# Performance work log

Measured on AMD Instinct MI355X. Metric: run time of the kernel, lower is better.

The kernel has to match this reference:

```python
import jax, jax.numpy as jnp
import numpy as np

N_NODES = 48758
REL_NUM = 5
BN_EPS = 1e-5


def _dan(h, edge_index, edge_type, win_w, win_b, wrel, cout_w, cout_b):
    # One DAN layer: gather -> gcn-norm scatter-sum + per-relation transform -> scatter-softmax -> scatter-sum.
    dst, src = edge_index[0], edge_index[1]
    xlin = h @ win_w + win_b                         # [N, D]
    x_j = xlin[src]                                  # [E, D] per-edge gather
    # gcn_norm(edge_index, add_self_loops=False): deg over col (= edge_index[1])
    ones = jnp.ones(src.shape[0], xlin.dtype)
    deg = jax.ops.segment_sum(ones, src, num_segments=N_NODES)
    dis = jnp.where(deg > 0, 1.0 / jnp.sqrt(deg), 0.0)
    norm = dis[dst] * dis[src]                       # [E]
    msg_gcn = jax.ops.segment_sum(x_j * norm[:, None], dst, num_segments=N_NODES)
    # per-relation linear transform on edge messages (small fixed relation loop)
    res = jnp.zeros_like(x_j)
    for r in range(REL_NUM):
        res = res + jnp.where((edge_type == r)[:, None], x_j @ wrel[r], 0.0)
    # scatter-softmax over destination-node neighborhoods, per feature channel
    m = jax.ops.segment_max(res, dst, num_segments=N_NODES)      # [N, D]
    e = jnp.exp(res - m[dst])
    s = jax.ops.segment_sum(e, dst, num_segments=N_NODES)
    weig = e / s[dst]
    msg = jax.ops.segment_sum(res * weig, dst, num_segments=N_NODES)
    return (msg_gcn + 0.1 * jax.nn.relu(msg)) @ cout_w + cout_b


def setup_inputs() -> dict:
    key = jax.random.key(0)
    ks = jax.random.split(key, 18)
    D = 128
    E = 750000
    s = 0.05
    inp = {}
    inp['x'] = jax.random.normal(ks[0], (N_NODES, D), jnp.float32)
    inp['edge_index'] = jax.random.randint(ks[1], (2, E), 0, N_NODES)
    inp['edge_type'] = jax.random.randint(ks[2], (E,), 0, REL_NUM)
    inp['edge_weight'] = jax.random.uniform(ks[3], (E,), jnp.float32)
    inp['idx'] = jax.random.randint(ks[4], (4096,), 0, N_NODES)
    # input projection + batchnorm params
    inp['proj_w'] = jax.random.normal(ks[5], (D, D), jnp.float32) * s
    inp['proj_b'] = jnp.zeros((D,), jnp.float32)
    inp['bn_g'] = jnp.ones((D,), jnp.float32)
    inp['bn_b'] = jnp.zeros((D,), jnp.float32)
    # two DAN layers (hidden=output=128)
    inp['win0_w'] = jax.random.normal(ks[6], (D, D), jnp.float32) * s
    inp['win0_b'] = jnp.zeros((D,), jnp.float32)
    inp['wrel0'] = jax.random.normal(ks[7], (REL_NUM, D, D), jnp.float32) * s
    inp['cout0_w'] = jax.random.normal(ks[8], (D, D), jnp.float32) * s
    inp['cout0_b'] = jnp.zeros((D,), jnp.float32)
    inp['win1_w'] = jax.random.normal(ks[9], (D, D), jnp.float32) * s
    inp['win1_b'] = jnp.zeros((D,), jnp.float32)
    inp['wrel1'] = jax.random.normal(ks[10], (REL_NUM, D, D), jnp.float32) * s
    inp['cout1_w'] = jax.random.normal(ks[11], (D, D), jnp.float32) * s
    inp['cout1_b'] = jnp.zeros((D,), jnp.float32)
    return inp


def reference(x, edge_index, edge_type, edge_weight, idx,
              proj_w, proj_b, bn_g, bn_b,
              win0_w, win0_b, wrel0, cout0_w, cout0_b,
              win1_w, win1_b, wrel1, cout1_w, cout1_b):
    # proj -> BatchNorm1d (training-mode batch stats) -> relu
    h = x @ proj_w + proj_b
    mu = jnp.mean(h, axis=0)
    var = jnp.mean(jnp.square(h - mu), axis=0)
    h = (h - mu) / jnp.sqrt(var + BN_EPS) * bn_g + bn_b
    h = jax.nn.relu(h)
    h = _dan(h, edge_index, edge_type, win0_w, win0_b, wrel0, cout0_w, cout0_b)
    h = _dan(h, edge_index, edge_type, win1_w, win1_b, wrel1, cout1_w, cout1_b)
    h = jax.nn.gelu(h, approximate=False)  # dropout is identity for reference
    return h[idx]
```

## Files before the change

kernel.cpp:

```cpp
#include <hip/hip_runtime.h>

#define HIST_BPG 32
#define HIST_B   (HIST_BPG * 4)
#define HIST_MAXW 12288

__device__ inline float bf2f(unsigned short u) {
    return __uint_as_float(((unsigned)u) << 16);
}
__device__ inline unsigned short f2bf(float f) {
    unsigned u = __float_as_uint(f);
    u += 0x7fffu + ((u >> 16) & 1u);
    return (unsigned short)(u >> 16);
}

__device__ inline int xcd_swizzle(int bid, int n)
{
    const int NX = 8;
    int q = n / NX, r = n % NX;
    int xcd = bid % NX;
    int rank = bid / NX;
    return (xcd < r) ? xcd * (q + 1) + rank : r * (q + 1) + (xcd - r) * q + rank;
}

typedef __attribute__((ext_vector_type(8))) short short8v;
typedef __attribute__((ext_vector_type(4))) float f32x4;


__device__ __forceinline__
void gemmf32_body(const float* __restrict__ A, const float* __restrict__ W,
                  const float* __restrict__ bias, float* __restrict__ C,
                  unsigned short* __restrict__ Ct, int M, int tile)
{
    __shared__ float As[64][132];
    __shared__ float Ws[32][128];

    const int tid = threadIdx.x;
    const int row0 = tile * 64;

#pragma unroll
    for (int i = 0; i < 8; ++i) {
        int idx = tid + i * 256;
        int rr = idx >> 5;
        int cc = (idx & 31) << 2;
        int gr = row0 + rr;
        float4 v = make_float4(0.f, 0.f, 0.f, 0.f);
        if (gr < M) v = *reinterpret_cast<const float4*>(A + (size_t)gr * 128 + cc);
        *reinterpret_cast<float4*>(&As[rr][cc]) = v;
    }

    const int tx = tid & 15;
    const int ty = tid >> 4;
    float acc[4][8];
#pragma unroll
    for (int i = 0; i < 4; ++i)
#pragma unroll
        for (int j = 0; j < 8; ++j) acc[i][j] = 0.f;

    for (int kt = 0; kt < 4; ++kt) {
        __syncthreads();
#pragma unroll
        for (int i = 0; i < 4; ++i) {
            int idx = tid + i * 256;
            int rr = idx >> 5;
            int cc = (idx & 31) << 2;
            *reinterpret_cast<float4*>(&Ws[rr][cc]) =
                *reinterpret_cast<const float4*>(W + (size_t)(kt * 32 + rr) * 128 + cc);
        }
        __syncthreads();
#pragma unroll
        for (int kk = 0; kk < 32; ++kk) {
            const int k = kt * 32 + kk;
            float a0 = As[ty * 4 + 0][k];
            float a1 = As[ty * 4 + 1][k];
            float a2 = As[ty * 4 + 2][k];
            float a3 = As[ty * 4 + 3][k];
            float w[8];
#pragma unroll
            for (int j = 0; j < 8; ++j) w[j] = Ws[kk][tx + 16 * j];
#pragma unroll
            for (int j = 0; j < 8; ++j) {
                acc[0][j] = fmaf(a0, w[j], acc[0][j]);
                acc[1][j] = fmaf(a1, w[j], acc[1][j]);
                acc[2][j] = fmaf(a2, w[j], acc[2][j]);
                acc[3][j] = fmaf(a3, w[j], acc[3][j]);
            }
        }
    }

    float bb[8];
#pragma unroll
    for (int j = 0; j < 8; ++j) bb[j] = bias ? bias[tx + 16 * j] : 0.f;

#pragma unroll
    for (int i = 0; i < 4; ++i) {
        int gr = row0 + ty * 4 + i;
        if (gr >= M) continue;
#pragma unroll
        for (int j = 0; j < 8; ++j) {
            float v = acc[i][j] + bb[j];
            if (C)  C[(size_t)gr * 128 + tx + 16 * j] = v;
            if (Ct) Ct[(size_t)(tx + 16 * j) * 128 + gr] = f2bf(v);
        }
    }
}

__device__ __forceinline__
void mfmaw_body(const unsigned short* __restrict__ A,
                const unsigned short* __restrict__ Wmat,
                const float* __restrict__ bias,
                float* __restrict__ Cf, unsigned short* __restrict__ Cb,
                int M, int tile)
{
    __shared__ unsigned short Bs[16384];

    const int tid = threadIdx.x;
#pragma unroll
    for (int i = 0; i < 4; ++i) {
        int idx = tid + i * 512;
        uint4 v = *reinterpret_cast<const uint4*>(Wmat + (size_t)idx * 8);
        int row = idx >> 4;
        int j = idx & 15;
        int byte = row * 256 + ((j ^ (row & 15)) << 4);
        *reinterpret_cast<uint4*>(reinterpret_cast<char*>(Bs) + byte) = v;
    }

    const int wave = tid >> 6;
    const int lane = tid & 63;
    const int grp = lane >> 4;
    const int l16 = lane & 15;
    const int row = tile * 128 + wave * 16 + l16;
    const int rc = row < M ? row : M - 1;

    short8v a[4];
#pragma unroll
    for (int kt = 0; kt < 4; ++kt)
        a[kt] = *reinterpret_cast<const short8v*>(A + (size_t)rc * 128 + kt * 32 + grp * 8);

    __syncthreads();

    f32x4 acc[8] = {};
#pragma unroll
    for (int kt = 0; kt < 4; ++kt) {
        const int joff = kt * 4 + grp;
#pragma unroll
        for (int n = 0; n < 8; ++n) {
            int brow = 16 * n + l16;
            int byte = brow * 256 + ((joff ^ (brow & 15)) << 4);
            short8v b = *reinterpret_cast<const short8v*>(
                reinterpret_cast<const char*>(Bs) + byte);
            acc[n] = __builtin_amdgcn_mfma_f32_16x16x32_bf16(b, a[kt], acc[n], 0, 0, 0);
        }
    }

    if (row >= M) return;

    float4 bb[8];
#pragma unroll
    for (int n = 0; n < 8; ++n)
        bb[n] = bias ? *reinterpret_cast<const float4*>(bias + 16 * n + grp * 4)
                     : make_float4(0.f, 0.f, 0.f, 0.f);

#pragma unroll
    for (int n = 0; n < 8; ++n) {
        float v0 = acc[n][0] + bb[n].x;
        float v1 = acc[n][1] + bb[n].y;
        float v2 = acc[n][2] + bb[n].z;
        float v3 = acc[n][3] + bb[n].w;
        if (Cf) {
            *reinterpret_cast<float4*>(Cf + (size_t)row * 128 + 16 * n + grp * 4) =
                make_float4(v0, v1, v2, v3);
        }
        if (Cb) {
            unsigned u0 = (unsigned)f2bf(v0) | ((unsigned)f2bf(v1) << 16);
            unsigned u1 = (unsigned)f2bf(v2) | ((unsigned)f2bf(v3) << 16);
            *reinterpret_cast<uint2*>(Cb + (size_t)row * 128 + 16 * n + grp * 4) =
                make_uint2(u0, u1);
        }
    }
}

__device__ void fused_dispatch(const unsigned short* A, const unsigned short* Wt,
                               const float* biasbuf, unsigned short* Xb,
                               unsigned short* Yb, int base, int M, int nmats,
                               int bid, int nF)
{
    int w = xcd_swizzle(bid, nF);
    int m = w % nmats;
    int tile = w / nmats;
    unsigned short* out = (m == 0) ? Xb : Yb + (size_t)(m - 1) * (size_t)M * 128;
    mfmaw_body(A, Wt + (size_t)(base + m) * 16384,
               biasbuf + (size_t)(base + m) * 128, nullptr, out, M, tile);
}

__device__ void biasprod_body(const float* __restrict__ v, const float* __restrict__ W,
                              const float* __restrict__ add, float* __restrict__ out)
{
    int t = threadIdx.x;
    if (t >= 128) return;
    float s = add ? add[t] : 0.f;
    for (int j = 0; j < 128; ++j) s = fmaf(v[j], W[(size_t)j * 128 + t], s);
    out[t] = s;
}

__device__ void wtconv_body(const float* __restrict__ W, unsigned short* __restrict__ O)
{
    for (int i = threadIdx.x; i < 16384; i += 256) {
        int k = i >> 7, n = i & 127;
        O[(size_t)n * 128 + k] = f2bf(W[i]);
    }
}

__device__ void bn_stats_body(const float* __restrict__ h, float* __restrict__ sums,
                              int Nn, int b)
{
    const int c = threadIdx.x & 127;
    const int half = threadIdx.x >> 7;
    float s = 0.f, q = 0.f;
    for (int row = b * 2 + half; row < Nn; row += 512) {
        float v = h[(size_t)row * 128 + c];
        s += v;
        q += v * v;
    }
    __shared__ float ls[256], lq[256];
    ls[threadIdx.x] = s;
    lq[threadIdx.x] = q;
    __syncthreads();
    if (half == 0) {
        s += ls[threadIdx.x + 128];
        q += lq[threadIdx.x + 128];
        atomicAdd(&sums[c], s);
        atomicAdd(&sums[128 + c], q);
    }
}

__device__ void scan_block_sums_body(const int* __restrict__ cnt, int* __restrict__ bsum,
                                     int Nn, int b)
{
    __shared__ int sd[256];
    int tid = threadIdx.x;
    int i = b * 256 + tid;
    sd[tid] = i < Nn ? ((cnt[i] + 3) & ~3) : 0;
    __syncthreads();
#pragma unroll
    for (int s = 128; s > 0; s >>= 1) {
        if (tid < s) sd[tid] += sd[tid + s];
        __syncthreads();
    }
    if (tid == 0) bsum[b] = sd[0];
}

__device__ void scan_offsets_body(int* __restrict__ bsum, int nb)
{
    __shared__ int sd[256];
    int tid = threadIdx.x;
    int v = tid < nb ? bsum[tid] : 0;
    sd[tid] = v;
    __syncthreads();
    for (int d = 1; d < 256; d <<= 1) {
        int t = tid >= d ? sd[tid - d] : 0;
        __syncthreads();
        sd[tid] += t;
        __syncthreads();
    }
    if (tid < nb) bsum[tid] = sd[tid] - v;
}


__global__ __launch_bounds__(256)
void hist_kernel(const int* __restrict__ ei, unsigned* __restrict__ partial,
                 int Nn, int E, int WORDS, int HALFR)
{
    __shared__ unsigned sh[HIST_MAXW];
    const int hbid = blockIdx.x;
    const int g = hbid / HIST_BPG;
    const int j = hbid - g * HIST_BPG;

    for (int w = threadIdx.x; w < WORDS; w += 256) sh[w] = 0;
    __syncthreads();

    const int* col = (g < 2) ? (ei + E) : ei;
    const int base = (g & 1) * HALFR;
    const size_t e0 = (size_t)E * j / HIST_BPG;
    const size_t e1 = (size_t)E * (j + 1) / HIST_BPG;
    for (size_t e = e0 + threadIdx.x; e < e1; e += 256) {
        int n = col[e] - base;
        if ((unsigned)n < (unsigned)HALFR)
            atomicAdd(&sh[n >> 1], 1u << ((n & 1) * 16));
    }
    __syncthreads();

    unsigned* out = partial + (size_t)hbid * WORDS;
    for (int w = threadIdx.x; w < WORDS; w += 256) out[w] = sh[w];
}

__global__ __launch_bounds__(256)
void kprod1(const float* win0w, const float* win0b, const float* win1w, const float* win1b,
            const float* cout0w, const float* cout0b, const float* cout1w,
            const float* cout1b, const float* wrel0,
            const float* x, const float* proj_w, const float* proj_b,
            unsigned short* xb, float* WfA1, unsigned short* Wt, float* biasbuf,
            int nrel, size_t nx4)
{
    const int IA1 = 1 + nrel, IC1 = 2 + 2 * nrel, IPRJ = 3 + 2 * nrel;
    const int nProd = 1 + nrel;
    int bid = blockIdx.x;
    if (bid < 2 * nProd) {
        int p = bid >> 1, tile = bid & 1;
        if (p == 0)
            gemmf32_body(cout0w, win1w, nullptr, WfA1, Wt + (size_t)IA1 * 16384, 128, tile);
        else
            gemmf32_body(win0w, wrel0 + (size_t)(p - 1) * 16384, nullptr,
                         nullptr, Wt + (size_t)p * 16384, 128, tile);
        return;
    }
    bid -= 2 * nProd;
    if (bid < nProd) {
        if (bid == 0) biasprod_body(cout0b, win1w, win1b, biasbuf + (size_t)IA1 * 128);
        else biasprod_body(win0b, wrel0 + (size_t)(bid - 1) * 16384, nullptr,
                           biasbuf + (size_t)bid * 128);
        return;
    }
    bid -= nProd;
    if (bid == 0) { wtconv_body(win0w, Wt); return; }
    if (bid == 1) { wtconv_body(cout1w, Wt + (size_t)IC1 * 16384); return; }
    if (bid == 2) { wtconv_body(proj_w, Wt + (size_t)IPRJ * 16384); return; }
    if (bid == 3) {
        int t = threadIdx.x;
        if (t < 128) {
            biasbuf[t] = win0b[t];
            biasbuf[(size_t)IC1 * 128 + t] = cout1b[t];
            biasbuf[(size_t)IPRJ * 128 + t] = proj_b[t];
        }
        return;
    }
    size_t i = (size_t)(bid - 4) * 256 + threadIdx.x;
    if (i < nx4) {
        float4 v = reinterpret_cast<const float4*>(x)[i];
        ushort4 pk = make_ushort4(f2bf(v.x), f2bf(v.y), f2bf(v.z), f2bf(v.w));
        reinterpret_cast<ushort4*>(xb)[i] = pk;
    }
}

__global__ __launch_bounds__(512)
void kproj(const unsigned short* xb, const unsigned short* Wt, const float* biasbuf,
           float* h, int mat, int M)
{
    mfmaw_body(xb, Wt + (size_t)mat * 16384, biasbuf + (size_t)mat * 128,
               h, nullptr, M, blockIdx.x);
}

__global__ __launch_bounds__(256)
void k2_reduce_bnstats(const unsigned* __restrict__ partial, float* __restrict__ dis,
                       int* __restrict__ cnt, const float* __restrict__ h,
                       float* __restrict__ bnsums, int Nn, int WORDS, int HALFR, int nRed)
{
    int bid = blockIdx.x;
    if (bid < nRed) {
        int t = bid * 256 + threadIdx.x;
        if (t < 4 * WORDS) {
            int histo = t / (2 * WORDS);
            int rem = t - histo * 2 * WORDS;
            int half = rem / WORDS;
            int w = rem - half * WORDS;
            int g = histo * 2 + half;
            unsigned slo = 0, shi = 0;
            const unsigned* p = partial + (size_t)(g * HIST_BPG) * WORDS + w;
#pragma unroll 4
            for (int j = 0; j < HIST_BPG; ++j) {
                unsigned u = p[(size_t)j * WORDS];
                slo += u & 0xffffu;
                shi += u >> 16;
            }
            int n0 = half * HALFR + 2 * w;
            int n1 = n0 + 1;
            if (histo == 0) {
                if (n0 < Nn) dis[n0] = slo ? rsqrtf((float)slo) : 0.f;
                if (n1 < Nn) dis[n1] = shi ? rsqrtf((float)shi) : 0.f;
            } else {
                if (n0 < Nn) cnt[n0] = (int)slo;
                if (n1 < Nn) cnt[n1] = (int)shi;
            }
        }
        return;
    }
    bn_stats_body(h, bnsums, Nn, bid - nRed);
}

__global__ __launch_bounds__(256)
void k3_prod2_bnfin_scan1(const float* wrel1, const float* WfA1,
                          unsigned short* Wt, float* biasbuf, int nrel,
                          const float* __restrict__ sums, const float* __restrict__ g,
                          const float* __restrict__ b, float* __restrict__ sc,
                          const int* __restrict__ cnt, int* __restrict__ bsum, int Nn)
{
    const int IA1 = 1 + nrel, IB1 = 2 + nrel;
    int bid = blockIdx.x;
    if (bid < 2 * nrel) {
        int p = bid >> 1, tile = bid & 1;
        gemmf32_body(WfA1, wrel1 + (size_t)p * 16384, nullptr,
                     nullptr, Wt + (size_t)(IB1 + p) * 16384, 128, tile);
        return;
    }
    bid -= 2 * nrel;
    if (bid < nrel) {
        biasprod_body(biasbuf + (size_t)IA1 * 128, wrel1 + (size_t)bid * 16384, nullptr,
                      biasbuf + (size_t)(IB1 + bid) * 128);
        return;
    }
    bid -= nrel;
    if (bid == 0) {
        int c = threadIdx.x;
        if (c < 128) {
            float inv = 1.f / (float)Nn;
            float mu = sums[c] * inv;
            float var = sums[128 + c] * inv - mu * mu;
            float rstd = rsqrtf(var + 1e-5f);
            float scale = rstd * g[c];
            sc[c] = scale;
            sc[128 + c] = b[c] - mu * scale;
        }
        return;
    }
    scan_block_sums_body(cnt, bsum, Nn, bid - 1);
}

__global__ __launch_bounds__(256)
void k4_scanoff_bnapply(int* __restrict__ bsum, int nb,
                        const float* __restrict__ h, const float* __restrict__ sc,
                        unsigned short* __restrict__ hb, size_t n4)
{
    if (blockIdx.x == 0) { scan_offsets_body(bsum, nb); return; }
    size_t i = (size_t)(blockIdx.x - 1) * 256 + threadIdx.x;
    if (i >= n4) return;
    int c = (int)(i & 31) << 2;
    float4 v = reinterpret_cast<const float4*>(h)[i];
    float o0 = fmaxf(fmaf(v.x, sc[c + 0], sc[128 + c + 0]), 0.f);
    float o1 = fmaxf(fmaf(v.y, sc[c + 1], sc[128 + c + 1]), 0.f);
    float o2 = fmaxf(fmaf(v.z, sc[c + 2], sc[128 + c + 2]), 0.f);
    float o3 = fmaxf(fmaf(v.w, sc[c + 3], sc[128 + c + 3]), 0.f);
    ushort4 pk = make_ushort4(f2bf(o0), f2bf(o1), f2bf(o2), f2bf(o3));
    reinterpret_cast<ushort4*>(hb)[i] = pk;
}

__global__ __launch_bounds__(256)
void k4b_scanfinal(const int* __restrict__ cnt, const int* __restrict__ bsum,
                   int* __restrict__ rowptr, int* __restrict__ cursor,
                   uint4* __restrict__ csr, unsigned* __restrict__ Yw,
                   unsigned sink_woff, int Nn, int nb)
{
    if ((int)blockIdx.x == nb) {
        int t = threadIdx.x;
        if (t < 64) Yw[sink_woff + t] = 0xC2C8C2C8u;
        return;
    }
    __shared__ int sd[256];
    int tid = threadIdx.x;
    int b = blockIdx.x;
    int i = b * 256 + tid;
    int v = i < Nn ? cnt[i] : 0;
    int pv = (v + 3) & ~3;
    sd[tid] = pv;
    __syncthreads();
    for (int d = 1; d < 256; d <<= 1) {
        int t2 = tid >= d ? sd[tid - d] : 0;
        __syncthreads();
        sd[tid] += t2;
        __syncthreads();
    }
    if (i < Nn) {
        int off = sd[tid] - pv + bsum[b];
        rowptr[i] = off;
        cursor[i] = off;
        uint4 sink = make_uint4(0u, sink_woff, 0u, 0u);
        for (int j = v; j < pv; ++j) csr[off + j] = sink;
        if (i == Nn - 1) {
            rowptr[Nn] = off + pv;
            for (int q = 0; q < 8; ++q) csr[off + pv + q] = sink;
        }
    }
}

__global__ __launch_bounds__(512)
void k5_mfma_scatter(const unsigned short* hb, const unsigned short* Wt,
                     const float* biasbuf, unsigned short* Xb, unsigned short* Yb,
                     int M, int nmats, int nF,
                     const int* __restrict__ ei, const int* __restrict__ et,
                     const float* __restrict__ dis, int* __restrict__ cursor,
                     uint4* __restrict__ csr, int E, int Nn, int nS)
{
    const int minv = nF < nS ? nF : nS;
    int bid = blockIdx.x;
    int fIdx = -1, sIdx = -1;
    if (bid < 2 * minv) {
        if (bid & 1) fIdx = bid >> 1; else sIdx = bid >> 1;
    } else {
        int rem = bid - 2 * minv;
        if (nF > nS) fIdx = minv + rem; else sIdx = minv + rem;
    }
    if (sIdx >= 0) {
        int e = sIdx * 512 + threadIdx.x;
        if (e < E) {
            int dst = ei[e];
            int src = ei[E + e];
            int pos = atomicAdd(&cursor[dst], 1);
            float nrm = dis[dst] * dis[src];
            csr[pos] = make_uint4((unsigned)(src * 64),
                                  (unsigned)((et[e] * Nn + src) * 64),
                                  __float_as_uint(nrm), 0u);
        }
        return;
    }
    fused_dispatch(hb, Wt, biasbuf, Xb, Yb, 0, M, nmats, fIdx, nF);
}

__global__ __launch_bounds__(512)
void k_fusedpass(const unsigned short* A, const unsigned short* Wt, const float* biasbuf,
                 unsigned short* Xb, unsigned short* Yb, int base, int M, int nmats,
                 int nF)
{
    fused_dispatch(A, Wt, biasbuf, Xb, Yb, base, M, nmats, blockIdx.x, nF);
}

__global__ __launch_bounds__(512)
void k_cout_gelu(const unsigned short* __restrict__ A, const unsigned short* Wt,
                 const float* biasbuf, float* __restrict__ out, int mat, int M)
{
    const unsigned short* Wmat = Wt + (size_t)mat * 16384;
    const float* bias = biasbuf + (size_t)mat * 128;

    __shared__ unsigned short Bs[16384];
    const int tid = threadIdx.x;
#pragma unroll
    for (int i = 0; i < 4; ++i) {
        int idx = tid + i * 512;
        uint4 v = *reinterpret_cast<const uint4*>(Wmat + (size_t)idx * 8);
        int row = idx >> 4;
        int j = idx & 15;
        int byte = row * 256 + ((j ^ (row & 15)) << 4);
        *reinterpret_cast<uint4*>(reinterpret_cast<char*>(Bs) + byte) = v;
    }

    const int wave = tid >> 6;
    const int lane = tid & 63;
    const int grp = lane >> 4;
    const int l16 = lane & 15;
    const int row = blockIdx.x * 128 + wave * 16 + l16;
    const int rc = row < M ? row : M - 1;

    short8v a[4];
#pragma unroll
    for (int kt = 0; kt < 4; ++kt)
        a[kt] = *reinterpret_cast<const short8v*>(A + (size_t)rc * 128 + kt * 32 + grp * 8);

    __syncthreads();

    f32x4 acc[8] = {};
#pragma unroll
    for (int kt = 0; kt < 4; ++kt) {
        const int joff = kt * 4 + grp;
#pragma unroll
        for (int n = 0; n < 8; ++n) {
            int brow = 16 * n + l16;
            int byte = brow * 256 + ((joff ^ (brow & 15)) << 4);
            short8v b = *reinterpret_cast<const short8v*>(
                reinterpret_cast<const char*>(Bs) + byte);
            acc[n] = __builtin_amdgcn_mfma_f32_16x16x32_bf16(b, a[kt], acc[n], 0, 0, 0);
        }
    }

    if (row >= M) return;

    const float kg = 0.7071067811865475f;
#pragma unroll
    for (int n = 0; n < 8; ++n) {
        float4 bb = *reinterpret_cast<const float4*>(bias + 16 * n + grp * 4);
        float v0 = acc[n][0] + bb.x;
        float v1 = acc[n][1] + bb.y;
        float v2 = acc[n][2] + bb.z;
        float v3 = acc[n][3] + bb.w;
        v0 = 0.5f * v0 * (1.f + erff(v0 * kg));
        v1 = 0.5f * v1 * (1.f + erff(v1 * kg));
        v2 = 0.5f * v2 * (1.f + erff(v2 * kg));
        v3 = 0.5f * v3 * (1.f + erff(v3 * kg));
        *reinterpret_cast<float4*>(out + (size_t)row * 128 + 16 * n + grp * 4) =
            make_float4(v0, v1, v2, v3);
    }
}

__global__ __launch_bounds__(256)
void node_gather(const int* __restrict__ rowptr, const uint4* __restrict__ csr,
                 const unsigned* __restrict__ Xw, const unsigned* __restrict__ Yw,
                 unsigned short* __restrict__ outb,
                 const int* __restrict__ idxmap, int count)
{
    int gid = blockIdx.x * 4 + (threadIdx.x >> 6);
    if (gid >= count) return;
    int node = idxmap ? idxmap[gid] : gid;
    int lane = threadIdx.x & 63;

    int i = rowptr[node];
    const int end = rowptr[node + 1];

    float mg0 = 0.f, mg1 = 0.f, s0 = 0.f, s1 = 0.f, t0 = 0.f, t1 = 0.f;

    if (i < end) {
        uint4 cur[4];
#pragma unroll
        for (int q = 0; q < 4; ++q) cur[q] = csr[i + q];

        for (; i < end; i += 4) {
            uint4 nxt[4];
#pragma unroll
            for (int q = 0; q < 4; ++q) nxt[q] = csr[i + 4 + q];

            unsigned xp[4], yp[4];
#pragma unroll
            for (int q = 0; q < 4; ++q) {
                xp[q] = Xw[cur[q].x + lane];
                yp[q] = Yw[cur[q].y + lane];
            }
#pragma unroll
            for (int q = 0; q < 4; ++q) {
                float nrm = __uint_as_float(cur[q].z);
                float x0 = bf2f((unsigned short)(xp[q] & 0xffffu));
                float x1 = bf2f((unsigned short)(xp[q] >> 16));
                float y0 = bf2f((unsigned short)(yp[q] & 0xffffu));
                float y1 = bf2f((unsigned short)(yp[q] >> 16));
                float w0 = __expf(y0), w1 = __expf(y1);
                mg0 = fmaf(x0, nrm, mg0);
                mg1 = fmaf(x1, nrm, mg1);
                s0 += w0; s1 += w1;
                t0 = fmaf(y0, w0, t0);
                t1 = fmaf(y1, w1, t1);
            }
#pragma unroll
            for (int q = 0; q < 4; ++q) cur[q] = nxt[q];
        }
    }

    float o0 = mg0 + 0.1f * fmaxf(s0 > 0.f ? t0 / s0 : 0.f, 0.f);
    float o1 = mg1 + 0.1f * fmaxf(s1 > 0.f ? t1 / s1 : 0.f, 0.f);
    unsigned pk = (unsigned)f2bf(o0) | ((unsigned)f2bf(o1) << 16);
    *reinterpret_cast<unsigned*>(outb + (size_t)gid * 128 + (lane << 1)) = pk;
}

extern "C" void kernel_launch(void* const* d_in, const int* in_sizes, int n_in,
                              void* d_out, int out_size, void* d_ws, size_t ws_size,
                              hipStream_t stream)
{
    const float* x      = (const float*)d_in[0];
    const int*   ei     = (const int*)d_in[1];
    const int*   et     = (const int*)d_in[2];
    const int*   idxp   = (const int*)d_in[4];
    const float* proj_w = (const float*)d_in[5];
    const float* proj_b = (const float*)d_in[6];
    const float* bn_g   = (const float*)d_in[7];
    const float* bn_b   = (const float*)d_in[8];
    const float* win_w[2]  = {(const float*)d_in[9],  (const float*)d_in[14]};
    const float* win_b[2]  = {(const float*)d_in[10], (const float*)d_in[15]};
    const float* wrel[2]   = {(const float*)d_in[11], (const float*)d_in[16]};
    const float* cout_w[2] = {(const float*)d_in[12], (const float*)d_in[17]};
    const float* cout_b[2] = {(const float*)d_in[13], (const float*)d_in[18]};

    const int Nn  = in_sizes[0] / 128;
    const int E   = in_sizes[1] / 2;
    const int Mo  = in_sizes[4];
    const int nrel = in_sizes[11] / (128 * 128);
    const size_t ND = (size_t)Nn * 128;

    const int HALFR = ((Nn + 3) / 4) * 2;
    const int WORDS = HALFR / 2;
    if (WORDS > HIST_MAXW) return;

    const int IA1 = 1 + nrel;
    const int IC1 = 2 + 2 * nrel;
    const int IPRJ = 3 + 2 * nrel;
    const int NMATS = 4 + 2 * nrel;

    char* p = (char*)d_ws;
    float* h    = (float*)p;                  p += ND * 4;
    unsigned short* hb = (unsigned short*)p;  p += ND * 2;
    unsigned short* xb = (unsigned short*)p;  p += ND * 2;
    unsigned short* Xb = (unsigned short*)p;  p += ND * 2;
    unsigned short* Yb = (unsigned short*)p;  p += (size_t)nrel * ND * 2 + 256;
    unsigned short* msgb = (unsigned short*)p; p += ND * 2;
    unsigned short* Wt = (unsigned short*)p;  p += (size_t)NMATS * 16384 * 2;
    float* WfA1 = (float*)p;                  p += (size_t)16384 * 4;
    float* biasbuf = (float*)p;               p += (size_t)NMATS * 128 * 4;
    uint4* csr  = (uint4*)p;                  p += ((size_t)E + 3 * (size_t)Nn + 16) * 16;
    unsigned* partial = (unsigned*)p;         p += (size_t)HIST_B * WORDS * 4;
    float* dis  = (float*)p;                  p += (size_t)Nn * 4;
    int*   cnt  = (int*)p;                    p += (size_t)Nn * 4;
    int*   rowptr = (int*)p;                  p += ((size_t)Nn + 1) * 4;
    int*   cursor = (int*)p;                  p += (size_t)Nn * 4;
    int*   bsum = (int*)p;                    p += 1024 * 4;
    float* bnsums = (float*)p;                p += 256 * 4;
    float* bnsc   = (float*)p;                p += 256 * 4;
    if ((size_t)(p - (char*)d_ws) > ws_size) return;

    const unsigned sink_woff = (unsigned)((size_t)nrel * Nn * 64);

    const int tiles128 = (Nn + 127) / 128;
    const size_t n4 = ND / 4;
    const int n4grid = (int)((n4 + 255) / 256);
    const int nb = (Nn + 255) / 256;
    const int nRed = (4 * WORDS + 255) / 256;
    const int nS = (E + 511) / 512;
    const int nmats = 1 + nrel;
    const int nFused = nmats * tiles128;
    const int nConv = (int)((n4 + 255) / 256);

    hipMemsetAsync(bnsums, 0, 256 * 4, stream);

    hist_kernel<<<HIST_B, 256, 0, stream>>>(ei, partial, Nn, E, WORDS, HALFR);

    kprod1<<<2 * (1 + nrel) + (1 + nrel) + 4 + nConv, 256, 0, stream>>>(
        win_w[0], win_b[0], win_w[1], win_b[1], cout_w[0], cout_b[0],
        cout_w[1], cout_b[1], wrel[0], x, proj_w, proj_b,
        xb, WfA1, Wt, biasbuf, nrel, n4);

    kproj<<<tiles128, 512, 0, stream>>>(xb, Wt, biasbuf, h, IPRJ, Nn);

    k2_reduce_bnstats<<<nRed + 256, 256, 0, stream>>>(
        partial, dis, cnt, h, bnsums, Nn, WORDS, HALFR, nRed);

    k3_prod2_bnfin_scan1<<<3 * nrel + 1 + nb, 256, 0, stream>>>(
        wrel[1], WfA1, Wt, biasbuf, nrel,
        bnsums, bn_g, bn_b, bnsc, cnt, bsum, Nn);

    k4_scanoff_bnapply<<<1 + n4grid, 256, 0, stream>>>(bsum, nb, h, bnsc, hb, n4);

    k4b_scanfinal<<<nb + 1, 256, 0, stream>>>(cnt, bsum, rowptr, cursor, csr,
                                              (unsigned*)Yb, sink_woff, Nn, nb);

    k5_mfma_scatter<<<nFused + nS, 512, 0, stream>>>(
        hb, Wt, biasbuf, Xb, Yb, Nn, nmats, nFused,
        ei, et, dis, cursor, csr, E, Nn, nS);

    node_gather<<<(Nn + 3) / 4, 256, 0, stream>>>(
        rowptr, csr, (const unsigned*)Xb, (const unsigned*)Yb, msgb, nullptr, Nn);

    k_fusedpass<<<nFused, 512, 0, stream>>>(msgb, Wt, biasbuf, Xb, Yb, IA1, Nn,
                                            nmats, nFused);

    node_gather<<<(Mo + 3) / 4, 256, 0, stream>>>(
        rowptr, csr, (const unsigned*)Xb, (const unsigned*)Yb, msgb, idxp, Mo);

    k_cout_gelu<<<(Mo + 127) / 128, 512, 0, stream>>>(
        msgb, Wt, biasbuf, (float*)d_out, IC1, Mo);
}
```

Before: 291.9 us.

## Interleave relation outputs per node, use exp2 with prescaled weights, fuse hist reduce

The per-relation Y outputs are stored interleaved per source node ([src][rel][128]) instead of relation-major, and the CSR offsets are updated to match. This is meant to improve locality when node_gather reads messages. Relation weights and biases are prescaled by log2(e) so the gather can use exp2f, with a ln2 factor applied at the output. The histogram reduction moves into the projection kernel launch, separate from the BN stats pass, which changes launch grouping.

```diff
diff --git a/kernel.cpp b/kernel.cpp
--- a/kernel.cpp
+++ b/kernel.cpp
@@ -3,6 +3,8 @@
 #define HIST_BPG 32
 #define HIST_B   (HIST_BPG * 4)
 #define HIST_MAXW 12288
+#define LOG2E 1.4426950408889634f
+#define LN2   0.6931471805599453f
 
 __device__ inline float bf2f(unsigned short u) {
     return __uint_as_float(((unsigned)u) << 16);
@@ -29,7 +31,7 @@
 __device__ __forceinline__
 void gemmf32_body(const float* __restrict__ A, const float* __restrict__ W,
                   const float* __restrict__ bias, float* __restrict__ C,
-                  unsigned short* __restrict__ Ct, int M, int tile)
+                  unsigned short* __restrict__ Ct, int M, int tile, float scale)
 {
     __shared__ float As[64][132];
     __shared__ float Ws[32][128];
@@ -97,7 +99,7 @@
         if (gr >= M) continue;
 #pragma unroll
         for (int j = 0; j < 8; ++j) {
-            float v = acc[i][j] + bb[j];
+            float v = (acc[i][j] + bb[j]) * scale;
             if (C)  C[(size_t)gr * 128 + tx + 16 * j] = v;
             if (Ct) Ct[(size_t)(tx + 16 * j) * 128 + gr] = f2bf(v);
         }
@@ -109,7 +111,7 @@
                 const unsigned short* __restrict__ Wmat,
                 const float* __restrict__ bias,
                 float* __restrict__ Cf, unsigned short* __restrict__ Cb,
-                int M, int tile)
+                int ldcb, int M, int tile)
 {
     __shared__ unsigned short Bs[16384];
 
@@ -173,7 +175,7 @@
         if (Cb) {
             unsigned u0 = (unsigned)f2bf(v0) | ((unsigned)f2bf(v1) << 16);
             unsigned u1 = (unsigned)f2bf(v2) | ((unsigned)f2bf(v3) << 16);
-            *reinterpret_cast<uint2*>(Cb + (size_t)row * 128 + 16 * n + grp * 4) =
+            *reinterpret_cast<uint2*>(Cb + (size_t)row * ldcb + 16 * n + grp * 4) =
                 make_uint2(u0, u1);
         }
     }
@@ -187,19 +189,21 @@
     int w = xcd_swizzle(bid, nF);
     int m = w % nmats;
     int tile = w / nmats;
-    unsigned short* out = (m == 0) ? Xb : Yb + (size_t)(m - 1) * (size_t)M * 128;
+    unsigned short* out = (m == 0) ? Xb : Yb + (size_t)(m - 1) * 128;
+    int ldcb = (m == 0) ? 128 : (nmats - 1) * 128;
     mfmaw_body(A, Wt + (size_t)(base + m) * 16384,
-               biasbuf + (size_t)(base + m) * 128, nullptr, out, M, tile);
+               biasbuf + (size_t)(base + m) * 128, nullptr, out, ldcb, M, tile);
 }
 
 __device__ void biasprod_body(const float* __restrict__ v, const float* __restrict__ W,
-                              const float* __restrict__ add, float* __restrict__ out)
+                              const float* __restrict__ add, float* __restrict__ out,
+                              float scale)
 {
     int t = threadIdx.x;
     if (t >= 128) return;
     float s = add ? add[t] : 0.f;
     for (int j = 0; j < 128; ++j) s = fmaf(v[j], W[(size_t)j * 128 + t], s);
-    out[t] = s;
+    out[t] = s * scale;
 }
 
 __device__ void wtconv_body(const float* __restrict__ W, unsigned short* __restrict__ O)
@@ -307,17 +311,18 @@
     if (bid < 2 * nProd) {
         int p = bid >> 1, tile = bid & 1;
         if (p == 0)
-            gemmf32_body(cout0w, win1w, nullptr, WfA1, Wt + (size_t)IA1 * 16384, 128, tile);
+            gemmf32_body(cout0w, win1w, nullptr, WfA1, Wt + (size_t)IA1 * 16384,
+                         128, tile, 1.f);
         else
             gemmf32_body(win0w, wrel0 + (size_t)(p - 1) * 16384, nullptr,
-                         nullptr, Wt + (size_t)p * 16384, 128, tile);
+                         nullptr, Wt + (size_t)p * 16384, 128, tile, LOG2E);
         return;
     }
     bid -= 2 * nProd;
     if (bid < nProd) {
-        if (bid == 0) biasprod_body(cout0b, win1w, win1b, biasbuf + (size_t)IA1 * 128);
+        if (bid == 0) biasprod_body(cout0b, win1w, win1b, biasbuf + (size_t)IA1 * 128, 1.f);
         else biasprod_body(win0b, wrel0 + (size_t)(bid - 1) * 16384, nullptr,
-                           biasbuf + (size_t)bid * 128);
+                           biasbuf + (size_t)bid * 128, LOG2E);
         return;
     }
     bid -= nProd;
@@ -342,48 +347,47 @@
 }
 
 __global__ __launch_bounds__(512)
-void kproj(const unsigned short* xb, const unsigned short* Wt, const float* biasbuf,
-           float* h, int mat, int M)
-{
-    mfmaw_body(xb, Wt + (size_t)mat * 16384, biasbuf + (size_t)mat * 128,
-               h, nullptr, M, blockIdx.x);
+void kproj_reduce(const unsigned short* xb, const unsigned short* Wt,
+                  const float* biasbuf, float* h, int mat, int M, int tiles,
+                  const unsigned* __restrict__ partial, float* __restrict__ dis,
+                  int* __restrict__ cnt, int Nn, int WORDS, int HALFR)
+{
+    if ((int)blockIdx.x < tiles) {
+        mfmaw_body(xb, Wt + (size_t)mat * 16384, biasbuf + (size_t)mat * 128,
+                   h, nullptr, 128, M, blockIdx.x);
+        return;
+    }
+    int t = (blockIdx.x - tiles) * 512 + threadIdx.x;
+    if (t < 4 * WORDS) {
+        int histo = t / (2 * WORDS);
+        int rem = t - histo * 2 * WORDS;
+        int half = rem / WORDS;
+        int w = rem - half * WORDS;
+        int g = histo * 2 + half;
+        unsigned slo = 0, shi = 0;
+        const unsigned* p = partial + (size_t)(g * HIST_BPG) * WORDS + w;
+#pragma unroll 4
+        for (int j = 0; j < HIST_BPG; ++j) {
+            unsigned u = p[(size_t)j * WORDS];
+            slo += u & 0xffffu;
+            shi += u >> 16;
+        }
+        int n0 = half * HALFR + 2 * w;
+        int n1 = n0 + 1;
+        if (histo == 0) {
+            if (n0 < Nn) dis[n0] = slo ? rsqrtf((float)slo) : 0.f;
+            if (n1 < Nn) dis[n1] = shi ? rsqrtf((float)shi) : 0.f;
+        } else {
+            if (n0 < Nn) cnt[n0] = (int)slo;
+            if (n1 < Nn) cnt[n1] = (int)shi;
+        }
+    }
 }
 
 __global__ __launch_bounds__(256)
-void k2_reduce_bnstats(const unsigned* __restrict__ partial, float* __restrict__ dis,
-                       int* __restrict__ cnt, const float* __restrict__ h,
-                       float* __restrict__ bnsums, int Nn, int WORDS, int HALFR, int nRed)
-{
-    int bid = blockIdx.x;
-    if (bid < nRed) {
-        int t = bid * 256 + threadIdx.x;
-        if (t < 4 * WORDS) {
-            int histo = t / (2 * WORDS);
-            int rem = t - histo * 2 * WORDS;
-            int half = rem / WORDS;
-            int w = rem - half * WORDS;
-            int g = histo * 2 + half;
-            unsigned slo = 0, shi = 0;
-            const unsigned* p = partial + (size_t)(g * HIST_BPG) * WORDS + w;
-#pragma unroll 4
-            for (int j = 0; j < HIST_BPG; ++j) {
-                unsigned u = p[(size_t)j * WORDS];
-                slo += u & 0xffffu;
-                shi += u >> 16;
-            }
-            int n0 = half * HALFR + 2 * w;
-            int n1 = n0 + 1;
-            if (histo == 0) {
-                if (n0 < Nn) dis[n0] = slo ? rsqrtf((float)slo) : 0.f;
-                if (n1 < Nn) dis[n1] = shi ? rsqrtf((float)shi) : 0.f;
-            } else {
-                if (n0 < Nn) cnt[n0] = (int)slo;
-                if (n1 < Nn) cnt[n1] = (int)shi;
-            }
-        }
-        return;
-    }
-    bn_stats_body(h, bnsums, Nn, bid - nRed);
+void k2_bnstats(const float* __restrict__ h, float* __restrict__ bnsums, int Nn)
+{
+    bn_stats_body(h, bnsums, Nn, blockIdx.x);
 }
 
 __global__ __launch_bounds__(256)
@@ -398,13 +402,13 @@
     if (bid < 2 * nrel) {
         int p = bid >> 1, tile = bid & 1;
         gemmf32_body(WfA1, wrel1 + (size_t)p * 16384, nullptr,
-                     nullptr, Wt + (size_t)(IB1 + p) * 16384, 128, tile);
+                     nullptr, Wt + (size_t)(IB1 + p) * 16384, 128, tile, LOG2E);
         return;
     }
     bid -= 2 * nrel;
     if (bid < nrel) {
         biasprod_body(biasbuf + (size_t)IA1 * 128, wrel1 + (size_t)bid * 16384, nullptr,
-                      biasbuf + (size_t)(IB1 + bid) * 128);
+                      biasbuf + (size_t)(IB1 + bid) * 128, LOG2E);
         return;
     }
     bid -= nrel;
@@ -488,6 +492,7 @@
                      const float* __restrict__ dis, int* __restrict__ cursor,
                      uint4* __restrict__ csr, int E, int Nn, int nS)
 {
+    const int nrel = nmats - 1;
     const int minv = nF < nS ? nF : nS;
     int bid = blockIdx.x;
     int fIdx = -1, sIdx = -1;
@@ -505,7 +510,7 @@
             int pos = atomicAdd(&cursor[dst], 1);
             float nrm = dis[dst] * dis[src];
             csr[pos] = make_uint4((unsigned)(src * 64),
-                                  (unsigned)((et[e] * Nn + src) * 64),
+                                  (unsigned)((src * nrel + et[e]) * 64),
                                   __float_as_uint(nrm), 0u);
         }
         return;
@@ -626,7 +631,7 @@
                 float x1 = bf2f((unsigned short)(xp[q] >> 16));
                 float y0 = bf2f((unsigned short)(yp[q] & 0xffffu));
                 float y1 = bf2f((unsigned short)(yp[q] >> 16));
-                float w0 = __expf(y0), w1 = __expf(y1);
+                float w0 = exp2f(y0), w1 = exp2f(y1);
                 mg0 = fmaf(x0, nrm, mg0);
                 mg1 = fmaf(x1, nrm, mg1);
                 s0 += w0; s1 += w1;
@@ -638,8 +643,8 @@
         }
     }
 
-    float o0 = mg0 + 0.1f * fmaxf(s0 > 0.f ? t0 / s0 : 0.f, 0.f);
-    float o1 = mg1 + 0.1f * fmaxf(s1 > 0.f ? t1 / s1 : 0.f, 0.f);
+    float o0 = mg0 + 0.1f * LN2 * fmaxf(s0 > 0.f ? t0 / s0 : 0.f, 0.f);
+    float o1 = mg1 + 0.1f * LN2 * fmaxf(s1 > 0.f ? t1 / s1 : 0.f, 0.f);
     unsigned pk = (unsigned)f2bf(o0) | ((unsigned)f2bf(o1) << 16);
     *reinterpret_cast<unsigned*>(outb + (size_t)gid * 128 + (lane << 1)) = pk;
 }
@@ -704,7 +709,7 @@
     const size_t n4 = ND / 4;
     const int n4grid = (int)((n4 + 255) / 256);
     const int nb = (Nn + 255) / 256;
-    const int nRed = (4 * WORDS + 255) / 256;
+    const int nRed512 = (4 * WORDS + 511) / 512;
     const int nS = (E + 511) / 512;
     const int nmats = 1 + nrel;
     const int nFused = nmats * tiles128;
@@ -719,10 +724,11 @@
         cout_w[1], cout_b[1], wrel[0], x, proj_w, proj_b,
         xb, WfA1, Wt, biasbuf, nrel, n4);
 
-    kproj<<<tiles128, 512, 0, stream>>>(xb, Wt, biasbuf, h, IPRJ, Nn);
-
-    k2_reduce_bnstats<<<nRed + 256, 256, 0, stream>>>(
-        partial, dis, cnt, h, bnsums, Nn, WORDS, HALFR, nRed);
+    kproj_reduce<<<tiles128 + nRed512, 512, 0, stream>>>(
+        xb, Wt, biasbuf, h, IPRJ, Nn, tiles128,
+        partial, dis, cnt, Nn, WORDS, HALFR);
+
+    k2_bnstats<<<256, 256, 0, stream>>>(h, bnsums, Nn);
 
     k3_prod2_bnfin_scan1<<<3 * nrel + 1 + nb, 256, 0, stream>>>(
         wrel[1], WfA1, Wt, biasbuf, nrel,
```

New measurement: 293.7 us. About the same (+0.6%).
